# Kernel tuning notes

Hardware: AMD Instinct MI355X
Metric: run time of the kernel (lower is better)

Reference implementation:

```python
import jax, jax.numpy as jnp
import numpy as np

D_HIDDEN = 1024
NUM_HEADS = 16
D_HEAD = D_HIDDEN // NUM_HEADS


def setup_inputs() -> dict:
    key = jax.random.key(0)
    ks = jax.random.split(key, 9)
    N, S, D = 4, 2048, D_HIDDEN
    s = 1.0 / np.sqrt(D)
    inp = {
        "x": jax.random.normal(ks[0], (N, S, D), dtype=jnp.float32),
        "Wq": jax.random.uniform(ks[1], (D, D), jnp.float32, -s, s),
        "bq": jnp.zeros((D,), jnp.float32),
        "Wk": jax.random.uniform(ks[2], (D, D), jnp.float32, -s, s),
        "bk": jnp.zeros((D,), jnp.float32),
        "Wv": jax.random.uniform(ks[3], (D, D), jnp.float32, -s, s),
        "bv": jnp.zeros((D,), jnp.float32),
        "Wo": jax.random.uniform(ks[4], (D, D), jnp.float32, -s, s),
        "bo": jnp.zeros((D,), jnp.float32),
        "ln_gamma": jnp.ones((D,), jnp.float32),
        "ln_beta": jnp.zeros((D,), jnp.float32),
    }
    return inp


def _layer_norm(x, gamma, beta, eps=1e-5):
    mu = jnp.mean(x, axis=-1, keepdims=True)
    var = jnp.var(x, axis=-1, keepdims=True)
    return (x - mu) * jax.lax.rsqrt(var + eps) * gamma + beta


def reference(x, Wq, bq, Wk, bk, Wv, bv, Wo, bo, ln_gamma, ln_beta):
    N, S, D = x.shape
    H, Dh = NUM_HEADS, D_HEAD
    xn = _layer_norm(x, ln_gamma, ln_beta)
    # torch Linear: y = x @ W.T + b
    q = (xn @ Wq.T + bq).reshape(N, S, H, Dh)
    k = (xn @ Wk.T + bk).reshape(N, S, H, Dh)
    v = (xn @ Wv.T + bv).reshape(N, S, H, Dh)
    # scores: [N, H, S, S]
    scores = jnp.einsum('nxhd,nyhd->nhxy', q, k) / np.sqrt(Dh)
    # causal mask: positions y > x get -inf
    mask = jnp.triu(jnp.full((S, S), -jnp.inf, dtype=scores.dtype), k=1)
    attn = jax.nn.softmax(scores + mask[None, None], axis=-1)
    z = jnp.einsum('nhxy,nyhd->nxhd', attn, v).reshape(N, S, D)
    return z @ Wo.T + bo
```

## Files before the change

kernel.cpp:

```cpp
#include <hip/hip_runtime.h>

typedef unsigned short u16;
typedef unsigned int   u32;
typedef __bf16 bf16x8 __attribute__((ext_vector_type(8)));
typedef float  f32x4  __attribute__((ext_vector_type(4)));
typedef unsigned short u16x8 __attribute__((ext_vector_type(8)));
typedef unsigned short u16x4 __attribute__((ext_vector_type(4)));

#define SEQ 2048
#define DM  1024
#define TOKS 8388608
#define SCLQ 0.18033688f

__device__ __forceinline__ float bf2f(u16 u) {
    u32 i = ((u32)u) << 16;
    float f; __builtin_memcpy(&f, &i, 4); return f;
}
__device__ __forceinline__ u16 f2bf(float f) {
    u32 i; __builtin_memcpy(&i, &f, 4);
    return (u16)((i + 0x7FFFu + ((i >> 16) & 1u)) >> 16);
}
__device__ __forceinline__ bf16x8 ld8(const u16* p) {
    return __builtin_bit_cast(bf16x8, *(const u16x8*)p);
}
#define GLD16(src, dst) __builtin_amdgcn_global_load_lds( \
    (const __attribute__((address_space(1))) void*)(src), \
    (__attribute__((address_space(3))) void*)(dst), 16, 0, 0)

#define SBAR() do { asm volatile("" ::: "memory"); __builtin_amdgcn_sched_barrier(0); \
    __builtin_amdgcn_s_barrier(); __builtin_amdgcn_sched_barrier(0); asm volatile("" ::: "memory"); } while (0)
#define WVM(n) asm volatile("s_waitcnt vmcnt(" #n ")" ::: "memory")
#define LGKM0() do { asm volatile("s_waitcnt lgkmcnt(0)" ::: "memory"); \
    __builtin_amdgcn_sched_barrier(0); } while (0)

__global__ __launch_bounds__(64) void detect_k(const u32* __restrict__ x, int* __restrict__ flag) {
    const int lane = threadIdx.x;
    u32 w = x[lane];
    int e0 = (int)((w >> 7) & 0xFFu);
    int cnt = (e0 >= 100 && e0 <= 140) ? 1 : 0;
#pragma unroll
    for (int off = 32; off; off >>= 1) cnt += __shfl_xor(cnt, off);
    if (lane == 0) *flag = (cnt < 32) ? 1 : 0;
}

__global__ __launch_bounds__(256) void convert_k(const void* s0, const void* s1, const void* s2, const void* s3,
                                                 const void* v0, const void* v1, const void* v2, const void* v3,
                                                 const void* v4, const void* v5,
                                                 u16* __restrict__ dstW, u16* __restrict__ dstV,
                                                 const int* __restrict__ flagp) {
    const int y = blockIdx.y, tid = threadIdx.x;
    const int fp32m = *flagp;
    const void* src; u16* dst; size_t off;
    if (y < 4) {
        src = (y == 0) ? s0 : (y == 1) ? s1 : (y == 2) ? s2 : s3;
        dst = dstW + (size_t)y * 1048576;
        off = (size_t)blockIdx.x * 1024 + tid * 4;
    } else {
        const int i = blockIdx.x;
        if (i >= 6) return;
        src = (i == 0) ? v0 : (i == 1) ? v1 : (i == 2) ? v2 : (i == 3) ? v3 : (i == 4) ? v4 : v5;
        dst = dstV + (size_t)i * 1024;
        off = (size_t)tid * 4;
    }
    u16x4 o;
    if (fp32m) {
        const float* f = (const float*)src + off;
#pragma unroll
        for (int j = 0; j < 4; ++j) o[j] = f2bf(f[j]);
    } else {
        o = *(const u16x4*)((const u16*)src + off);
    }
    *(u16x4*)(dst + off) = o;
}

__global__ __launch_bounds__(256) void ln_k(const void* __restrict__ xv,
                                            const u16* __restrict__ g,
                                            const u16* __restrict__ b,
                                            u16* __restrict__ xn,
                                            const int* __restrict__ flagp) {
    const int row = blockIdx.x, tid = threadIdx.x;
    const int fp32m = *flagp;
    float f[4], s1 = 0.f, s2 = 0.f;
    if (fp32m) {
        f32x4 v = *(const f32x4*)((const float*)xv + (size_t)row * DM + tid * 4);
#pragma unroll
        for (int j = 0; j < 4; ++j) f[j] = v[j];
    } else {
        u16x4 v = *(const u16x4*)((const u16*)xv + (size_t)row * DM + tid * 4);
#pragma unroll
        for (int j = 0; j < 4; ++j) f[j] = bf2f(v[j]);
    }
#pragma unroll
    for (int j = 0; j < 4; ++j) { s1 += f[j]; s2 += f[j] * f[j]; }
#pragma unroll
    for (int off = 32; off; off >>= 1) { s1 += __shfl_xor(s1, off); s2 += __shfl_xor(s2, off); }
    __shared__ float red[8];
    const int wave = tid >> 6, lane = tid & 63;
    if (lane == 0) { red[wave] = s1; red[4 + wave] = s2; }
    __syncthreads();
    s1 = red[0] + red[1] + red[2] + red[3];
    s2 = red[4] + red[5] + red[6] + red[7];
    const float mu = s1 * (1.f / DM);
    const float var = s2 * (1.f / DM) - mu * mu;
    const float rs = rsqrtf(var + 1e-5f);
    u16x4 gv = *(const u16x4*)(g + tid * 4);
    u16x4 bv = *(const u16x4*)(b + tid * 4);
    u16x4 o;
#pragma unroll
    for (int j = 0; j < 4; ++j) o[j] = f2bf((f[j] - mu) * rs * bf2f(gv[j]) + bf2f(bv[j]));
    *(u16x4*)(xn + (size_t)row * DM + tid * 4) = o;
}

__global__ __launch_bounds__(512, 2) void gemm_qkv_k(const u16* __restrict__ xn, const u16* __restrict__ Wc,
                                                     const u16* __restrict__ Vc,
                                                     u16* __restrict__ Q, u16* __restrict__ K, u16* __restrict__ Vt) {
    __shared__ alignas(16) u16 lds[65536];
    const int tid = threadIdx.x;
    const int w = tid >> 6, lane = tid & 63;
    const int l4 = lane & 15, q4 = lane >> 4;
    const int bm = blockIdx.x, bn = blockIdx.y;
    const int wm0 = (w >> 2) * 128, wn = (w & 3) * 64;

    const int srow = lane >> 3, schk = (lane & 7) ^ srow;
    const u16* aS = xn + ((size_t)(bm * 256) + srow) * DM + schk * 8;
    const u16* bS = Wc + ((size_t)(bn * 256) + srow) * DM + schk * 8;
    const int rb = w * 16;

    auto STG = [&](int kind, int ut) {
        const int slotb = kind * 16384 + (ut & 1) * 8192;
        int g0;
        if (kind == 0)      g0 = (rb < 64) ? rb : rb + 64;
        else if (kind == 1) g0 = (rb < 64) ? rb + 64 : rb + 128;
        else if (kind == 2) g0 = rb;
        else                g0 = rb + 128;
        const u16* src = (kind < 2 ? aS : bS) + (size_t)g0 * DM + (size_t)ut * 64;
        u16* dst = lds + slotb + rb * 64;
        GLD16(src, dst);
        GLD16(src + 8 * DM, dst + 512);
    };

    const int swz0 = (q4 ^ (l4 & 7)) << 3;
    const int swz1 = ((4 + q4) ^ (l4 & 7)) << 3;
    const int arow = ((w >> 2) * 64 + l4) * 64;
    const int bbase = (wn & 127);
    const int brow = (bbase + l4) * 64;
    const int bsel = (w & 2) ? 49152 : 32768;

    f32x4 acc[8][4] = {};
    bf16x8 af[4], b0r[4], b1r[4];

    STG(0, 0); STG(2, 0); STG(3, 0); STG(1, 0); STG(0, 1); STG(2, 1);
    WVM(6);
    SBAR();

#pragma unroll 2
    for (int u = 0; u < 16; ++u) {
        const int sb = (u & 1) * 8192;
        const u16* AE = lds + sb;
        const u16* AO = lds + 16384 + sb;
        const u16* BB = lds + bsel + sb;
#pragma unroll
        for (int mt = 0; mt < 4; ++mt) af[mt] = ld8(AE + arow + mt * 1024 + swz0);
#pragma unroll
        for (int nt = 0; nt < 4; ++nt) b0r[nt] = ld8(BB + brow + nt * 1024 + swz0);
        if (u < 15) STG(3, u + 1);
        SBAR(); LGKM0();
        __builtin_amdgcn_s_setprio(1);
#pragma unroll
        for (int mt = 0; mt < 4; ++mt)
#pragma unroll
            for (int nt = 0; nt < 4; ++nt)
                acc[mt][nt] = __builtin_amdgcn_mfma_f32_16x16x32_bf16(af[mt], b0r[nt], acc[mt][nt], 0, 0, 0);
        __builtin_amdgcn_s_setprio(0);
        SBAR();
#pragma unroll
        for (int mt = 0; mt < 4; ++mt) af[mt] = ld8(AE + arow + mt * 1024 + swz1);
#pragma unroll
        for (int nt = 0; nt < 4; ++nt) b1r[nt] = ld8(BB + brow + nt * 1024 + swz1);
        if (u < 15) STG(1, u + 1);
        if (u < 15) { WVM(8); } else { WVM(0); }
        SBAR(); LGKM0();
        __builtin_amdgcn_s_setprio(1);
#pragma unroll
        for (int mt = 0; mt < 4; ++mt)
#pragma unroll
            for (int nt = 0; nt < 4; ++nt)
                acc[mt][nt] = __builtin_amdgcn_mfma_f32_16x16x32_bf16(af[mt], b1r[nt], acc[mt][nt], 0, 0, 0);
        __builtin_amdgcn_s_setprio(0);
        SBAR();
#pragma unroll
        for (int mt = 0; mt < 4; ++mt) af[mt] = ld8(AO + arow + mt * 1024 + swz0);
        if (u < 14) STG(0, u + 2);
        SBAR(); LGKM0();
        __builtin_amdgcn_s_setprio(1);
#pragma unroll
        for (int mt = 0; mt < 4; ++mt)
#pragma unroll
            for (int nt = 0; nt < 4; ++nt)
                acc[mt + 4][nt] = __builtin_amdgcn_mfma_f32_16x16x32_bf16(af[mt], b0r[nt], acc[mt + 4][nt], 0, 0, 0);
        __builtin_amdgcn_s_setprio(0);
        SBAR();
#pragma unroll
        for (int mt = 0; mt < 4; ++mt) af[mt] = ld8(AO + arow + mt * 1024 + swz1);
        if (u < 14) STG(2, u + 2);
        if (u < 14) { WVM(6); } else if (u == 14) { WVM(2); } else { WVM(0); }
        SBAR(); LGKM0();
        __builtin_amdgcn_s_setprio(1);
#pragma unroll
        for (int mt = 0; mt < 4; ++mt)
#pragma unroll
            for (int nt = 0; nt < 4; ++nt)
                acc[mt + 4][nt] = __builtin_amdgcn_mfma_f32_16x16x32_bf16(af[mt], b1r[nt], acc[mt + 4][nt], 0, 0, 0);
        __builtin_amdgcn_s_setprio(0);
        SBAR();
    }

    const int whichB = bn >> 2;
    const int cb = (bn & 3) * 256 + wn;
    u16* outp = (whichB == 0) ? Q : (whichB == 1) ? K : Vt;
    const float scl = (whichB == 0) ? SCLQ : 1.0f;
    float bs4[4];
#pragma unroll
    for (int nt = 0; nt < 4; ++nt) bs4[nt] = bf2f(Vc[whichB * 1024 + cb + nt * 16 + l4]);
    if (whichB < 2) {
#pragma unroll
        for (int mt = 0; mt < 8; ++mt) {
            const int row0 = bm * 256 + wm0 + mt * 16 + q4 * 4;
#pragma unroll
            for (int r = 0; r < 4; ++r) {
                u16* rowp = outp + (size_t)(row0 + r) * DM + cb;
#pragma unroll
                for (int nt = 0; nt < 4; ++nt)
                    rowp[nt * 16 + l4] = f2bf((acc[mt][nt][r] + bs4[nt]) * scl);
            }
        }
    } else {
#pragma unroll
        for (int nt = 0; nt < 4; ++nt) {
            const int cc = cb + nt * 16 + l4;
#pragma unroll
            for (int mt = 0; mt < 8; ++mt) {
                const int row0 = bm * 256 + wm0 + mt * 16 + q4 * 4;
                const int nbk = row0 >> 11, s0 = row0 & 2047;
                u16x4 pk;
#pragma unroll
                for (int r = 0; r < 4; ++r) pk[r] = f2bf(acc[mt][nt][r] + bs4[nt]);
                *(u16x4*)(outp + ((size_t)(nbk * 1024 + cc)) * SEQ + s0) = pk;
            }
        }
    }
}

#define LDS_U16 73728

__device__ __forceinline__ void wait_vm12() { asm volatile("s_waitcnt vmcnt(12)" ::: "memory"); }
__device__ __forceinline__ void wait_vm6()  { asm volatile("s_waitcnt vmcnt(6)"  ::: "memory"); }
__device__ __forceinline__ void wait_vm0()  { asm volatile("s_waitcnt vmcnt(0)"  ::: "memory"); }

__device__ __forceinline__ void gemm256x128_out(u16* lds,
                                                const u16* __restrict__ A,
                                                const u16* __restrict__ W,
                                                const u16* __restrict__ bias,
                                                u16* __restrict__ o0,
                                                int fp32m) {
    const int tid = threadIdx.x;
    const int w = tid >> 6, lane = tid & 63;
    const int l4 = lane & 15, q4 = lane >> 4;
    const int bm = blockIdx.x, bn = blockIdx.y;
    const int wm = (w >> 1) * 64, wn = (w & 1) * 64;

    const int srow = lane >> 3;
    const int schk = (lane & 7) ^ srow;
    const u16* sA = A + ((size_t)(bm * 256 + w * 32 + srow)) * DM + (schk << 3);
    const u16* sB = W + ((size_t)(bn * 128 + w * 16 + srow)) * DM + (schk << 3);

    int offA[4][2], offB[4][2];
#pragma unroll
    for (int mt = 0; mt < 4; ++mt)
#pragma unroll
        for (int s = 0; s < 2; ++s) {
            const int row = wm + mt * 16 + l4;
            offA[mt][s] = row * 64 + (((s * 4 + q4) ^ (l4 & 7)) << 3);
        }
#pragma unroll
    for (int nt = 0; nt < 4; ++nt)
#pragma unroll
        for (int s = 0; s < 2; ++s) {
            const int row = wn + nt * 16 + l4;
            offB[nt][s] = 16384 + row * 64 + (((s * 4 + q4) ^ (l4 & 7)) << 3);
        }

    auto STAGE = [&](int kt, int b) {
        const u16* a0 = sA + kt * 64;
        const u16* b0 = sB + kt * 64;
        u16* la = lds + b * 24576 + w * 2048;
        u16* lb = lds + b * 24576 + 16384 + w * 1024;
        GLD16(a0,           la);
        GLD16(a0 + 8 * DM,  la + 512);
        GLD16(a0 + 16 * DM, la + 1024);
        GLD16(a0 + 24 * DM, la + 1536);
        GLD16(b0,           lb);
        GLD16(b0 + 8 * DM,  lb + 512);
    };

    f32x4 acc[4][4] = {};

    STAGE(0, 0); STAGE(1, 1); STAGE(2, 2);

#pragma unroll 4
    for (int kt = 0; kt < 16; ++kt) {
        const int b = kt % 3;
        if (kt < 14)      wait_vm12();
        else if (kt == 14) wait_vm6();
        else               wait_vm0();
        __builtin_amdgcn_s_barrier();
        __builtin_amdgcn_sched_barrier(0);
        const u16* base = lds + b * 24576;
        bf16x8 af[4][2], bfr[4][2];
#pragma unroll
        for (int mt = 0; mt < 4; ++mt)
#pragma unroll
            for (int s = 0; s < 2; ++s) af[mt][s] = ld8(base + offA[mt][s]);
#pragma unroll
        for (int nt = 0; nt < 2; ++nt)
#pragma unroll
            for (int s = 0; s < 2; ++s) bfr[nt][s] = ld8(base + offB[nt][s]);
        __builtin_amdgcn_s_setprio(1);
#pragma unroll
        for (int mt = 0; mt < 4; ++mt)
#pragma unroll
            for (int nt = 0; nt < 2; ++nt)
#pragma unroll
                for (int s = 0; s < 2; ++s)
                    acc[mt][nt] = __builtin_amdgcn_mfma_f32_16x16x32_bf16(af[mt][s], bfr[nt][s], acc[mt][nt], 0, 0, 0);
        __builtin_amdgcn_s_setprio(0);
#pragma unroll
        for (int nt = 2; nt < 4; ++nt)
#pragma unroll
            for (int s = 0; s < 2; ++s) bfr[nt][s] = ld8(base + offB[nt][s]);
        __builtin_amdgcn_s_setprio(1);
#pragma unroll
        for (int mt = 0; mt < 4; ++mt)
#pragma unroll
            for (int nt = 2; nt < 4; ++nt)
#pragma unroll
                for (int s = 0; s < 2; ++s)
                    acc[mt][nt] = __builtin_amdgcn_mfma_f32_16x16x32_bf16(af[mt][s], bfr[nt][s], acc[mt][nt], 0, 0, 0);
        __builtin_amdgcn_s_setprio(0);
        __builtin_amdgcn_s_barrier();
        __builtin_amdgcn_sched_barrier(0);
        if (kt < 13) STAGE(kt + 3, b);
    }

#pragma unroll
    for (int nt = 0; nt < 4; ++nt) {
        const int cc = bn * 128 + wn + nt * 16 + l4;
        const float bs = bf2f(bias[cc]);
#pragma unroll
        for (int mt = 0; mt < 4; ++mt) {
            const int row0 = bm * 256 + wm + mt * 16 + q4 * 4;
            if (fp32m) {
#pragma unroll
                for (int r = 0; r < 4; ++r)
                    ((float*)o0)[(size_t)(row0 + r) * DM + cc] = acc[mt][nt][r] + bs;
            } else {
#pragma unroll
                for (int r = 0; r < 4; ++r)
                    o0[(size_t)(row0 + r) * DM + cc] = f2bf(acc[mt][nt][r] + bs);
            }
        }
    }
}

__global__ __launch_bounds__(512, 2) void gemm_out_k(const u16* __restrict__ Z, const u16* __restrict__ Wc,
                                                     const u16* __restrict__ Vc,
                                                     u16* __restrict__ out, const int* __restrict__ flagp) {
    __shared__ alignas(16) u16 lds[LDS_U16];
    const int fp32m = *flagp;
    gemm256x128_out(lds, Z, Wc + 3 * 1048576, Vc + 3 * 1024, out, fp32m);
}

__global__ __launch_bounds__(256, 4) void flash_k(const u16* __restrict__ Q,
                                                  const u16* __restrict__ K,
                                                  const u16* __restrict__ Vt,
                                                  u16* __restrict__ Z) {
    const int bh = blockIdx.x;
    const int qb = 15 - (int)blockIdx.y;
    const int n = bh >> 4, h = bh & 15;
    const int tid = threadIdx.x, wave = tid >> 6, lane = tid & 63;
    const int l4 = lane & 15, q4 = lane >> 4;

    __shared__ alignas(16) u16 Ks[2][64 * 32];
    __shared__ alignas(16) u16 Vs[2][64 * 32];
    __shared__ alignas(16) u16 Pl[4][2][16 * 72];

    const int Q0w = qb * 128 + wave * 32;
    bf16x8 qf[2][2];
#pragma unroll
    for (int qt = 0; qt < 2; ++qt) {
        const u16* Qr = Q + ((size_t)(n * SEQ + Q0w + qt * 16 + l4)) * DM + h * 64 + q4 * 8;
        qf[qt][0] = ld8(Qr);
        qf[qt][1] = ld8(Qr + 32);
    }

    const int srow = lane >> 2, scol = (lane & 3) * 8;
    const u16* Kg = K + ((size_t)(n * SEQ + wave * 16 + srow)) * DM + h * 64 + scol;
    const u16* Vg = Vt + ((size_t)(n * 1024 + h * 64 + wave * 16 + srow)) * SEQ + scol;
    u16* KsD0 = &Ks[0][wave * 512];
    u16* KsD1 = &Ks[1][wave * 512];
    u16* VsD0 = &Vs[0][wave * 512];
    u16* VsD1 = &Vs[1][wave * 512];

    f32x4 o[2][4] = {};
    float l_acc[2] = {0.f, 0.f};
    const int nch = 2 * qb + 2;

    for (int c = 0; c < nch; ++c) {
        const int kv0 = c * 64;
        const size_t krow = (size_t)kv0 * DM;
        GLD16(Kg + krow, KsD0);
        GLD16(Kg + krow + 32, KsD1);
        GLD16(Vg + kv0, VsD0);
        GLD16(Vg + kv0 + 32, VsD1);
        __syncthreads();

        bf16x8 a[4][2];
#pragma unroll
        for (int mt = 0; mt < 4; ++mt) {
            a[mt][0] = ld8(&Ks[0][(mt * 16 + l4) * 32 + q4 * 8]);
            a[mt][1] = ld8(&Ks[1][(mt * 16 + l4) * 32 + q4 * 8]);
        }
#pragma unroll
        for (int qt = 0; qt < 2; ++qt) {
            f32x4 st[4];
#pragma unroll
            for (int mt = 0; mt < 4; ++mt) {
                f32x4 zz = {0.f, 0.f, 0.f, 0.f};
                st[mt] = __builtin_amdgcn_mfma_f32_16x16x32_bf16(a[mt][0], qf[qt][0], zz, 0, 0, 0);
                st[mt] = __builtin_amdgcn_mfma_f32_16x16x32_bf16(a[mt][1], qf[qt][1], st[mt], 0, 0, 0);
            }
            const int qg = Q0w + qt * 16 + l4;
            u16* P = Pl[wave][qt];
            float la = l_acc[qt];
#pragma unroll
            for (int mt = 0; mt < 4; ++mt) {
                __bf16 pk[4];
#pragma unroll
                for (int r = 0; r < 4; ++r) {
                    const int kv = kv0 + mt * 16 + q4 * 4 + r;
                    float p = __builtin_amdgcn_exp2f(st[mt][r]);
                    p = (kv > qg) ? 0.f : p;
                    la += p;
                    pk[r] = (__bf16)p;
                }
                *(u16x4*)(P + l4 * 72 + mt * 16 + q4 * 4) = *(u16x4*)pk;
            }
            l_acc[qt] = la;
        }
#pragma unroll
        for (int ks = 0; ks < 2; ++ks) {
            bf16x8 pf0 = ld8(&Pl[wave][0][l4 * 72 + ks * 32 + q4 * 8]);
            bf16x8 pf1 = ld8(&Pl[wave][1][l4 * 72 + ks * 32 + q4 * 8]);
#pragma unroll
            for (int nt = 0; nt < 4; ++nt) {
                bf16x8 vf = ld8(&Vs[ks][(nt * 16 + l4) * 32 + q4 * 8]);
                o[0][nt] = __builtin_amdgcn_mfma_f32_16x16x32_bf16(pf0, vf, o[0][nt], 0, 0, 0);
                o[1][nt] = __builtin_amdgcn_mfma_f32_16x16x32_bf16(pf1, vf, o[1][nt], 0, 0, 0);
            }
        }
        __syncthreads();
    }

#pragma unroll
    for (int qt = 0; qt < 2; ++qt) {
        float l = l_acc[qt];
        l += __shfl_xor(l, 16);
        l += __shfl_xor(l, 32);
        float lr[4];
#pragma unroll
        for (int r = 0; r < 4; ++r) lr[r] = 1.f / __shfl(l, q4 * 4 + r);
#pragma unroll
        for (int nt = 0; nt < 4; ++nt) {
            const int col = h * 64 + nt * 16 + l4;
#pragma unroll
            for (int r = 0; r < 4; ++r) {
                const int row = n * SEQ + Q0w + qt * 16 + q4 * 4 + r;
                Z[(size_t)row * DM + col] = f2bf(o[qt][nt][r] * lr[r]);
            }
        }
    }
}

extern "C" void kernel_launch(void* const* d_in, const int* in_sizes, int n_in,
                              void* d_out, int out_size, void* d_ws, size_t ws_size,
                              hipStream_t stream) {
    const void* x  = d_in[0];
    const void* Wq = d_in[1];
    const void* bq = d_in[2];
    const void* Wk = d_in[3];
    const void* bk = d_in[4];
    const void* Wv = d_in[5];
    const void* bv = d_in[6];
    const void* Wo = d_in[7];
    const void* bo = d_in[8];
    const void* g  = d_in[9];
    const void* b  = d_in[10];
    u16* ws = (u16*)d_ws;

    u16* xn  = ws;
    u16* Qb  = ws + (size_t)TOKS;
    u16* Kb  = ws + (size_t)2 * TOKS;
    u16* Vtb = ws + (size_t)3 * TOKS;
    u16* Zb  = ws;
    u16* Wc  = ws + (size_t)4 * TOKS;
    u16* Vc  = Wc + 4 * 1048576;
    int* flagp = (int*)(Vc + 8 * 1024);

    detect_k<<<dim3(1), 64, 0, stream>>>((const u32*)x, flagp);
    convert_k<<<dim3(1024, 5), 256, 0, stream>>>(Wq, Wk, Wv, Wo, bq, bk, bv, bo, g, b, Wc, Vc, flagp);
    ln_k<<<dim3(4 * SEQ), 256, 0, stream>>>(x, Vc + 4 * 1024, Vc + 5 * 1024, xn, flagp);
    gemm_qkv_k<<<dim3(32, 12), 512, 0, stream>>>(xn, Wc, Vc, Qb, Kb, Vtb);
    flash_k<<<dim3(64, 16), 256, 0, stream>>>(Qb, Kb, Vtb, Zb);
    gemm_out_k<<<dim3(32, 8), 512, 0, stream>>>(Zb, Wc, Vc, (u16*)d_out, flagp);
}
```

Measured before the change: 257.4 us.

## Swizzle flash K/V LDS tiles and drop sched barriers around GEMM barriers

In the flash attention kernel, the K and V tiles move from two 32-column half buffers to a single 64-column XOR-swizzled LDS layout. Each lane now loads a full 128-byte row segment per global-to-LDS copy, and the fragment reads apply the same swizzle to avoid bank conflicts. In the QKV GEMM, the sched_barrier fences around s_barrier are removed so the compiler can schedule instructions across the barriers. This risks the compiler moving LDS reads or MFMAs in ways that hurt the intended interleaving.

Result: no change. 252.5 us (-1.9%).

```diff
diff --git a/kernel.cpp b/kernel.cpp
--- a/kernel.cpp
+++ b/kernel.cpp
@@ -27,8 +27,8 @@
     (const __attribute__((address_space(1))) void*)(src), \
     (__attribute__((address_space(3))) void*)(dst), 16, 0, 0)
 
-#define SBAR() do { asm volatile("" ::: "memory"); __builtin_amdgcn_sched_barrier(0); \
-    __builtin_amdgcn_s_barrier(); __builtin_amdgcn_sched_barrier(0); asm volatile("" ::: "memory"); } while (0)
+#define BARX() do { asm volatile("" ::: "memory"); __builtin_amdgcn_s_barrier(); \
+    asm volatile("" ::: "memory"); } while (0)
 #define WVM(n) asm volatile("s_waitcnt vmcnt(" #n ")" ::: "memory")
 #define LGKM0() do { asm volatile("s_waitcnt lgkmcnt(0)" ::: "memory"); \
     __builtin_amdgcn_sched_barrier(0); } while (0)
@@ -151,7 +151,7 @@
 
     STG(0, 0); STG(2, 0); STG(3, 0); STG(1, 0); STG(0, 1); STG(2, 1);
     WVM(6);
-    SBAR();
+    BARX();
 
 #pragma unroll 2
     for (int u = 0; u < 16; ++u) {
@@ -164,7 +164,7 @@
 #pragma unroll
         for (int nt = 0; nt < 4; ++nt) b0r[nt] = ld8(BB + brow + nt * 1024 + swz0);
         if (u < 15) STG(3, u + 1);
-        SBAR(); LGKM0();
+        BARX(); LGKM0();
         __builtin_amdgcn_s_setprio(1);
 #pragma unroll
         for (int mt = 0; mt < 4; ++mt)
@@ -172,14 +172,14 @@
             for (int nt = 0; nt < 4; ++nt)
                 acc[mt][nt] = __builtin_amdgcn_mfma_f32_16x16x32_bf16(af[mt], b0r[nt], acc[mt][nt], 0, 0, 0);
         __builtin_amdgcn_s_setprio(0);
-        SBAR();
+        BARX();
 #pragma unroll
         for (int mt = 0; mt < 4; ++mt) af[mt] = ld8(AE + arow + mt * 1024 + swz1);
 #pragma unroll
         for (int nt = 0; nt < 4; ++nt) b1r[nt] = ld8(BB + brow + nt * 1024 + swz1);
         if (u < 15) STG(1, u + 1);
         if (u < 15) { WVM(8); } else { WVM(0); }
-        SBAR(); LGKM0();
+        BARX(); LGKM0();
         __builtin_amdgcn_s_setprio(1);
 #pragma unroll
         for (int mt = 0; mt < 4; ++mt)
@@ -187,11 +187,11 @@
             for (int nt = 0; nt < 4; ++nt)
                 acc[mt][nt] = __builtin_amdgcn_mfma_f32_16x16x32_bf16(af[mt], b1r[nt], acc[mt][nt], 0, 0, 0);
         __builtin_amdgcn_s_setprio(0);
-        SBAR();
+        BARX();
 #pragma unroll
         for (int mt = 0; mt < 4; ++mt) af[mt] = ld8(AO + arow + mt * 1024 + swz0);
         if (u < 14) STG(0, u + 2);
-        SBAR(); LGKM0();
+        BARX(); LGKM0();
         __builtin_amdgcn_s_setprio(1);
 #pragma unroll
         for (int mt = 0; mt < 4; ++mt)
@@ -199,12 +199,12 @@
             for (int nt = 0; nt < 4; ++nt)
                 acc[mt + 4][nt] = __builtin_amdgcn_mfma_f32_16x16x32_bf16(af[mt], b0r[nt], acc[mt + 4][nt], 0, 0, 0);
         __builtin_amdgcn_s_setprio(0);
-        SBAR();
+        BARX();
 #pragma unroll
         for (int mt = 0; mt < 4; ++mt) af[mt] = ld8(AO + arow + mt * 1024 + swz1);
         if (u < 14) STG(2, u + 2);
         if (u < 14) { WVM(6); } else if (u == 14) { WVM(2); } else { WVM(0); }
-        SBAR(); LGKM0();
+        BARX(); LGKM0();
         __builtin_amdgcn_s_setprio(1);
 #pragma unroll
         for (int mt = 0; mt < 4; ++mt)
@@ -212,7 +212,7 @@
             for (int nt = 0; nt < 4; ++nt)
                 acc[mt + 4][nt] = __builtin_amdgcn_mfma_f32_16x16x32_bf16(af[mt], b1r[nt], acc[mt + 4][nt], 0, 0, 0);
         __builtin_amdgcn_s_setprio(0);
-        SBAR();
+        BARX();
     }
 
     const int whichB = bn >> 2;
@@ -390,8 +390,8 @@
     const int tid = threadIdx.x, wave = tid >> 6, lane = tid & 63;
     const int l4 = lane & 15, q4 = lane >> 4;
 
-    __shared__ alignas(16) u16 Ks[2][64 * 32];
-    __shared__ alignas(16) u16 Vs[2][64 * 32];
+    __shared__ alignas(16) u16 Ks[64 * 64];
+    __shared__ alignas(16) u16 Vs[64 * 64];
     __shared__ alignas(16) u16 Pl[4][2][16 * 72];
 
     const int Q0w = qb * 128 + wave * 32;
@@ -403,13 +403,11 @@
         qf[qt][1] = ld8(Qr + 32);
     }
 
-    const int srow = lane >> 2, scol = (lane & 3) * 8;
-    const u16* Kg = K + ((size_t)(n * SEQ + wave * 16 + srow)) * DM + h * 64 + scol;
-    const u16* Vg = Vt + ((size_t)(n * 1024 + h * 64 + wave * 16 + srow)) * SEQ + scol;
-    u16* KsD0 = &Ks[0][wave * 512];
-    u16* KsD1 = &Ks[1][wave * 512];
-    u16* VsD0 = &Vs[0][wave * 512];
-    u16* VsD1 = &Vs[1][wave * 512];
+    const int sr8 = lane >> 3, sc8 = (lane & 7) ^ (lane >> 3);
+    const u16* Kg = K + ((size_t)(n * SEQ + wave * 16 + sr8)) * DM + h * 64 + sc8 * 8;
+    const u16* Vg = Vt + ((size_t)(n * 1024 + h * 64 + wave * 16 + sr8)) * SEQ + sc8 * 8;
+    u16* KsD = Ks + wave * 1024;
+    u16* VsD = Vs + wave * 1024;
 
     f32x4 o[2][4] = {};
     float l_acc[2] = {0.f, 0.f};
@@ -418,17 +416,17 @@
     for (int c = 0; c < nch; ++c) {
         const int kv0 = c * 64;
         const size_t krow = (size_t)kv0 * DM;
-        GLD16(Kg + krow, KsD0);
-        GLD16(Kg + krow + 32, KsD1);
-        GLD16(Vg + kv0, VsD0);
-        GLD16(Vg + kv0 + 32, VsD1);
+        GLD16(Kg + krow,          KsD);
+        GLD16(Kg + krow + 8 * DM, KsD + 512);
+        GLD16(Vg + kv0,           VsD);
+        GLD16(Vg + kv0 + 8 * SEQ, VsD + 512);
         __syncthreads();
 
         bf16x8 a[4][2];
 #pragma unroll
         for (int mt = 0; mt < 4; ++mt) {
-            a[mt][0] = ld8(&Ks[0][(mt * 16 + l4) * 32 + q4 * 8]);
-            a[mt][1] = ld8(&Ks[1][(mt * 16 + l4) * 32 + q4 * 8]);
+            a[mt][0] = ld8(Ks + (mt * 16 + l4) * 64 + (((q4) ^ (l4 & 7)) << 3));
+            a[mt][1] = ld8(Ks + (mt * 16 + l4) * 64 + (((4 + q4) ^ (l4 & 7)) << 3));
         }
 #pragma unroll
         for (int qt = 0; qt < 2; ++qt) {
@@ -463,7 +461,7 @@
             bf16x8 pf1 = ld8(&Pl[wave][1][l4 * 72 + ks * 32 + q4 * 8]);
 #pragma unroll
             for (int nt = 0; nt < 4; ++nt) {
-                bf16x8 vf = ld8(&Vs[ks][(nt * 16 + l4) * 32 + q4 * 8]);
+                bf16x8 vf = ld8(Vs + (nt * 16 + l4) * 64 + (((ks * 4 + q4) ^ (l4 & 7)) << 3));
                 o[0][nt] = __builtin_amdgcn_mfma_f32_16x16x32_bf16(pf0, vf, o[0][nt], 0, 0, 0);
                 o[1][nt] = __builtin_amdgcn_mfma_f32_16x16x32_bf16(pf1, vf, o[1][nt], 0, 0, 0);
             }
```
